# Optimization experiments

Measured on AMD Instinct MI355X. Metric: run time of the kernel, lower is better.

The kernel has to match this reference:

```python
import jax, jax.numpy as jnp
import numpy as np

TOTAL = 819200   # total flattened labels
BATCH = 16384    # number of samples (segments)
DIM = 128        # embed_dim
LABELS_PER = 50  # constant segment length (TOTAL = BATCH * LABELS_PER)


def setup_inputs() -> dict:
    key = jax.random.key(0)
    k_emb, k_w1, k_b1, k_w2, k_b2 = jax.random.split(key, 5)
    embeddings = jax.random.normal(k_emb, (TOTAL, DIM), dtype=jnp.float32)
    # weight_net params (PyTorch nn.Linear default-ish init scale)
    s1 = 1.0 / np.sqrt(DIM)
    W1 = jax.random.uniform(k_w1, (DIM, DIM), jnp.float32, -s1, s1)
    b1 = jax.random.uniform(k_b1, (DIM,), jnp.float32, -s1, s1)
    W2 = jax.random.uniform(k_w2, (DIM, 1), jnp.float32, -s1, s1)
    b2 = jax.random.uniform(k_b2, (1,), jnp.float32, -s1, s1)
    lengths = jnp.full((BATCH,), LABELS_PER, dtype=jnp.int32)
    return {"embeddings": embeddings, "W1": W1, "b1": b1, "W2": W2, "b2": b2,
            "lengths": lengths}


def reference(embeddings, W1, b1, W2, b2, lengths):
    # MLP scorer: Linear -> ReLU -> Linear -> Softmax(dim=0) (GLOBAL over all labels)
    h = jnp.maximum(embeddings @ W1 + b1, 0.0)           # (T, D)
    scores = h @ W2 + b2                                  # (T, 1)
    weights = jax.nn.softmax(scores, axis=0)              # (T, 1) global softmax
    # Ragged per-segment weighted sum via segment_sum
    batch = lengths.shape[0]
    total = embeddings.shape[0]
    seg_ids = jnp.repeat(jnp.arange(batch, dtype=jnp.int32), lengths,
                         total_repeat_length=total)       # (T,)
    pooled = jax.ops.segment_sum(embeddings * weights, seg_ids,
                                 num_segments=batch)      # (B, D)
    return pooled
```

## Files before the change

kernel.cpp:

```cpp
#include <hip/hip_runtime.h>
#include <hip/hip_bf16.h>
#include <math.h>

#define DIM 128

typedef __attribute__((ext_vector_type(8))) short bf16x8;
typedef __attribute__((ext_vector_type(4))) float f32x4;

union FragU { bf16x8 v; __hip_bfloat162 h[4]; };

static __device__ __forceinline__ ushort f2bf(float f) {
    unsigned u = __float_as_uint(f);
    u += 0x7FFFu + ((u >> 16) & 1u);
    return (ushort)(u >> 16);
}

typedef __attribute__((address_space(1))) const unsigned GASp;
typedef __attribute__((address_space(3))) unsigned LASp;
static __device__ __forceinline__ void gll16(const void* g, void* l) {
    __builtin_amdgcn_global_load_lds((GASp*)g, (LASp*)l, 16, 0, 0);
}

static __device__ __forceinline__ void stage16(float* buf, const float* emb,
                                               long row0, long Tm1, int lane) {
    #pragma unroll
    for (int i = 0; i < 8; ++i) {
        int s = i * 64 + lane;
        int r = s >> 5, x = s & 31;
        long gr = row0 + r; gr = (gr > Tm1) ? Tm1 : gr;
        gll16(emb + gr * 128 + ((x ^ (r & 7)) << 2), (char*)buf + i * 1024);
    }
}

__global__ __launch_bounds__(1024) void scan_kernel(const int* __restrict__ lengths,
                                                    int* __restrict__ offsets, int batch,
                                                    int* __restrict__ uniflag) {
    __shared__ int tsum[1024];
    __shared__ int ok;
    int tid = threadIdx.x;
    if (tid == 0) ok = 1;
    int L0 = lengths[0];
    int per = (batch + 1023) >> 10;
    int start = tid * per;
    int s = 0;
    int loc = 1;
    for (int i = 0; i < per; ++i) {
        int idx = start + i;
        if (idx < batch) {
            int l = lengths[idx];
            s += l;
            if (l != L0) loc = 0;
        }
    }
    tsum[tid] = s;
    __syncthreads();
    if (!loc) atomicAnd(&ok, 0);
    for (int off = 1; off < 1024; off <<= 1) {
        int v = (tid >= off) ? tsum[tid - off] : 0;
        __syncthreads();
        tsum[tid] += v;
        __syncthreads();
    }
    int base = (tid == 0) ? 0 : tsum[tid - 1];
    for (int i = 0; i < per; ++i) {
        int idx = start + i;
        if (idx < batch) { offsets[idx] = base; base += lengths[idx]; }
    }
    __syncthreads();
    if (tid == 0) uniflag[0] = ok;
}

static __device__ __forceinline__ void chunk_body(
        const float* __restrict__ bufc, int cv, int lane, int lr, int lg,
        int xc, int xh, const bf16x8 (&bfrag)[8][4],
        const float (&b1r)[8], const float (&w2r)[8],
        float& r_ref, float& Sp, float& t0, float& t1) {
    bf16x8 a[4];
    #pragma unroll
    for (int kc = 0; kc < 4; ++kc) {
        int c0 = kc * 8 + lg * 2;
        float4 q0 = *(const float4*)&bufc[(lr * 32 + (c0 ^ (lr & 7))) * 4];
        float4 q1 = *(const float4*)&bufc[(lr * 32 + ((c0 + 1) ^ (lr & 7))) * 4];
        FragU f;
        f.h[0] = __float22bfloat162_rn(make_float2(q0.x, q0.y));
        f.h[1] = __float22bfloat162_rn(make_float2(q0.z, q0.w));
        f.h[2] = __float22bfloat162_rn(make_float2(q1.x, q1.y));
        f.h[3] = __float22bfloat162_rn(make_float2(q1.z, q1.w));
        a[kc] = f.v;
    }

    f32x4 acc[8];
    #pragma unroll
    for (int ct = 0; ct < 8; ++ct) acc[ct] = (f32x4)(0.f);
    #pragma unroll
    for (int ct = 0; ct < 8; ++ct)
        #pragma unroll
        for (int kc = 0; kc < 4; ++kc)
            acc[ct] = __builtin_amdgcn_mfma_f32_16x16x32_bf16(a[kc], bfrag[ct][kc], acc[ct], 0, 0, 0);

    float p[4];
    #pragma unroll
    for (int reg = 0; reg < 4; ++reg) {
        float s = 0.f;
        #pragma unroll
        for (int ct = 0; ct < 8; ++ct) {
            float h = acc[ct][reg] + b1r[ct];
            h = fmaxf(h, 0.f);
            s = fmaf(h, w2r[ct], s);
        }
        p[reg] = s;
    }
    #pragma unroll
    for (int m = 1; m < 16; m <<= 1) {
        #pragma unroll
        for (int reg = 0; reg < 4; ++reg)
            p[reg] += __shfl_xor(p[reg], m, 64);
    }
    int r3 = lane & 3;
    float pr = p[0];
    pr = (r3 == 1) ? p[1] : pr;
    pr = (r3 == 2) ? p[2] : pr;
    pr = (r3 == 3) ? p[3] : pr;
    int src = ((lane & 12) << 2) + r3;
    float sv = __shfl(pr, src, 64);

    float s_l = (lr < cv) ? sv : -INFINITY;

    if (!__all(s_l - r_ref <= 8.f)) {
        float m_c = s_l;
        #pragma unroll
        for (int o = 1; o < 16; o <<= 1) m_c = fmaxf(m_c, __shfl_xor(m_c, o, 64));
        float r_new = fmaxf(r_ref, m_c);
        float scl = __expf(r_ref - r_new);
        Sp *= scl; t0 *= scl; t1 *= scl;
        r_ref = r_new;
    }
    float w_l = __expf(s_l - r_ref);
    Sp += w_l;

    #pragma unroll
    for (int jg = 0; jg < 4; ++jg) {
        int j0 = jg * 4;
        float2 e0 = *(const float2*)&bufc[((j0 + 0) * 32 + (xc ^ ((j0 + 0) & 7))) * 4 + xh * 2];
        float2 e1 = *(const float2*)&bufc[((j0 + 1) * 32 + (xc ^ ((j0 + 1) & 7))) * 4 + xh * 2];
        float2 e2 = *(const float2*)&bufc[((j0 + 2) * 32 + (xc ^ ((j0 + 2) & 7))) * 4 + xh * 2];
        float2 e3 = *(const float2*)&bufc[((j0 + 3) * 32 + (xc ^ ((j0 + 3) & 7))) * 4 + xh * 2];
        float w0 = __uint_as_float(__builtin_amdgcn_readlane(__float_as_uint(w_l), j0 + 0));
        float w1v = __uint_as_float(__builtin_amdgcn_readlane(__float_as_uint(w_l), j0 + 1));
        float w2v = __uint_as_float(__builtin_amdgcn_readlane(__float_as_uint(w_l), j0 + 2));
        float w3 = __uint_as_float(__builtin_amdgcn_readlane(__float_as_uint(w_l), j0 + 3));
        t0 = fmaf(w0, e0.x, t0); t1 = fmaf(w0, e0.y, t1);
        t0 = fmaf(w1v, e1.x, t0); t1 = fmaf(w1v, e1.y, t1);
        t0 = fmaf(w2v, e2.x, t0); t1 = fmaf(w2v, e2.y, t1);
        t0 = fmaf(w3, e3.x, t0); t1 = fmaf(w3, e3.y, t1);
    }
}

__global__ __launch_bounds__(256, 2) void fused_kernel(
        const float* __restrict__ emb, const float* __restrict__ W1,
        const float* __restrict__ b1, const float* __restrict__ W2,
        const float* __restrict__ b2, const int* __restrict__ offsets,
        const int* __restrict__ lengths, int batch, int T,
        const int* __restrict__ uniflag,
        float* __restrict__ mArr, float* __restrict__ sArr,
        float* __restrict__ tvec) {
    __shared__ __align__(16) char smem[65536];

    int tid = threadIdx.x;
    int lane = tid & 63;
    int wv = tid >> 6;
    int lr = lane & 15;
    int lg = lane >> 4;

    ushort* sB = (ushort*)smem;
    for (int i = 0; i < 16; ++i) {
        int q = tid + i * 256;
        int n = q >> 5;
        int k4 = q & 31;
        ushort4 w;
        w.x = f2bf(W1[(k4 * 4 + 0) * DIM + n]);
        w.y = f2bf(W1[(k4 * 4 + 1) * DIM + n]);
        w.z = f2bf(W1[(k4 * 4 + 2) * DIM + n]);
        w.w = f2bf(W1[(k4 * 4 + 3) * DIM + n]);
        int c = k4 >> 1;
        int a16 = n * 128 + ((c ^ (n & 7)) * 8) + (k4 & 1) * 4;
        *(ushort4*)&sB[a16] = w;
    }
    __syncthreads();
    bf16x8 bfrag[8][4];
    #pragma unroll
    for (int ct = 0; ct < 8; ++ct) {
        int n = ct * 16 + lr;
        #pragma unroll
        for (int kc = 0; kc < 4; ++kc) {
            int c = lg + kc * 4;
            bfrag[ct][kc] = *(const bf16x8*)&sB[n * 128 + ((c ^ (n & 7)) * 8)];
        }
    }
    float b1r[8], w2r[8];
    #pragma unroll
    for (int ct = 0; ct < 8; ++ct) {
        b1r[ct] = b1[ct * 16 + lr];
        w2r[ct] = W2[ct * 16 + lr];
    }
    __syncthreads();

    float* buf0 = (float*)(smem + wv * 16384);
    float* buf1 = (float*)(smem + wv * 16384 + 8192);

    long Tm1 = (long)T - 1;
    int nwaves = gridDim.x * 4;
    int gwave = blockIdx.x * 4 + wv;
    int per = (batch + nwaves - 1) / nwaves;
    int seg0 = gwave * per;
    int segend = seg0 + per; if (segend > batch) segend = batch;
    if (seg0 >= segend) return;

    int xc = lane >> 1, xh = lane & 1;
    int uni = __builtin_amdgcn_readfirstlane(uniflag[0]);

    if (uni) {
        int L = __builtin_amdgcn_readfirstlane(lengths[0]);
        int nch = (L + 15) >> 4;
        int ss = seg0, sc = 0;
        #pragma unroll
        for (int k = 0; k < 2; ++k) {
            if (ss < segend) {
                stage16(k ? buf1 : buf0, emb, (long)ss * L + sc * 16, Tm1, lane);
                if (++sc == nch) { sc = 0; ++ss; }
            }
        }
        int cur = 0;
        for (int seg = seg0; seg < segend; ++seg) {
            float r_ref = -INFINITY, Sp = 0.f, t0 = 0.f, t1 = 0.f;
            for (int c = 0; c < nch; ++c) {
                if (seg == segend - 1 && c == nch - 1)
                    asm volatile("s_waitcnt vmcnt(0)" ::: "memory");
                else
                    asm volatile("s_waitcnt vmcnt(8)" ::: "memory");
                float* bufc = cur ? buf1 : buf0;
                chunk_body(bufc, L - c * 16, lane, lr, lg, xc, xh,
                           bfrag, b1r, w2r, r_ref, Sp, t0, t1);
                asm volatile("s_waitcnt lgkmcnt(0)" ::: "memory");
                if (ss < segend) {
                    stage16(bufc, emb, (long)ss * L + sc * 16, Tm1, lane);
                    if (++sc == nch) { sc = 0; ++ss; }
                }
                cur ^= 1;
            }
            #pragma unroll
            for (int o = 1; o < 16; o <<= 1) Sp += __shfl_xor(Sp, o, 64);
            *(float2*)&tvec[(long)seg * DIM + 2 * lane] = make_float2(t0, t1);
            if (lane == 0) { mArr[seg] = r_ref; sArr[seg] = Sp; }
        }
    } else {
        for (int seg = seg0; seg < segend; ++seg) {
            long off = offsets[seg];
            int len = lengths[seg];
            int nch = (len + 15) >> 4;
            float r_ref = -INFINITY, Sp = 0.f, t0 = 0.f, t1 = 0.f;

            if (nch > 0) stage16(buf0, emb, off, Tm1, lane);
            if (nch > 1) stage16(buf1, emb, off + 16, Tm1, lane);

            for (int c = 0; c < nch; ++c) {
                float* bufc = (c & 1) ? buf1 : buf0;
                if (c + 1 < nch) asm volatile("s_waitcnt vmcnt(8)" ::: "memory");
                else             asm volatile("s_waitcnt vmcnt(0)" ::: "memory");
                chunk_body(bufc, len - c * 16, lane, lr, lg, xc, xh,
                           bfrag, b1r, w2r, r_ref, Sp, t0, t1);
                asm volatile("s_waitcnt lgkmcnt(0)" ::: "memory");
                if (c + 2 < nch) stage16(bufc, emb, off + (long)(c + 2) * 16, Tm1, lane);
            }
            #pragma unroll
            for (int o = 1; o < 16; o <<= 1) Sp += __shfl_xor(Sp, o, 64);
            *(float2*)&tvec[(long)seg * DIM + 2 * lane] = make_float2(t0, t1);
            if (lane == 0) { mArr[seg] = r_ref; sArr[seg] = Sp; }
        }
    }
}

__global__ __launch_bounds__(1024) void segreduce_kernel(const float* __restrict__ mArr,
        const float* __restrict__ sArr, int batch, float* __restrict__ stats) {
    __shared__ float redm[16], reds[16];
    int tid = threadIdx.x;
    int wave = tid >> 6, ln = tid & 63;
    float m = -INFINITY;
    for (int i = tid; i < batch; i += 1024) m = fmaxf(m, mArr[i]);
    #pragma unroll
    for (int o = 32; o >= 1; o >>= 1) m = fmaxf(m, __shfl_xor(m, o, 64));
    if (ln == 0) redm[wave] = m;
    __syncthreads();
    float M = -INFINITY;
    #pragma unroll
    for (int k = 0; k < 16; ++k) M = fmaxf(M, redm[k]);
    float s = 0.f;
    for (int i = tid; i < batch; i += 1024) s += sArr[i] * expf(mArr[i] - M);
    #pragma unroll
    for (int o = 32; o >= 1; o >>= 1) s += __shfl_xor(s, o, 64);
    if (ln == 0) reds[wave] = s;
    __syncthreads();
    if (tid == 0) {
        float S = 0.f;
        #pragma unroll
        for (int k = 0; k < 16; ++k) S += reds[k];
        stats[0] = M;
        stats[1] = 1.0f / S;
    }
}

__global__ __launch_bounds__(256) void scale_kernel(const float* __restrict__ tvec,
        const float* __restrict__ mArr, const float* __restrict__ stats,
        float* __restrict__ out, int n) {
    int idx = blockIdx.x * 256 + threadIdx.x;
    if (idx >= n) return;
    float M = stats[0], invS = stats[1];
    int b = idx >> 7;
    out[idx] = tvec[idx] * (expf(mArr[b] - M) * invS);
}

extern "C" void kernel_launch(void* const* d_in, const int* in_sizes, int n_in,
                              void* d_out, int out_size, void* d_ws, size_t ws_size,
                              hipStream_t stream) {
    const float* emb     = (const float*)d_in[0];
    const float* W1      = (const float*)d_in[1];
    const float* b1      = (const float*)d_in[2];
    const float* W2      = (const float*)d_in[3];
    const float* b2      = (const float*)d_in[4];
    const int*   lengths = (const int*)d_in[5];
    int T = in_sizes[0] / DIM;
    int batch = in_sizes[5];
    float* out = (float*)d_out;

    int*   offsets = (int*)d_ws;
    float* mArr    = (float*)(offsets + batch);
    float* sArr    = mArr + batch;
    float* stats   = sArr + batch;
    int*   uniflag = (int*)(stats + 2);
    float* tvec    = stats + 4;

    scan_kernel<<<1, 1024, 0, stream>>>(lengths, offsets, batch, uniflag);
    fused_kernel<<<512, 256, 0, stream>>>(emb, W1, b1, W2, b2, offsets, lengths,
                                          batch, T, uniflag, mArr, sArr, tvec);
    segreduce_kernel<<<1, 1024, 0, stream>>>(mArr, sArr, batch, stats);
    scale_kernel<<<(out_size + 255) / 256, 256, 0, stream>>>(tvec, mArr, stats, out, out_size);
}
```

Before: 163.6 us.

## Pool from bf16 MFMA fragments in registers and prefetch next chunk earlier

Pooling now reuses the bf16 A-fragments already loaded for the MFMA and keeps a per-lane 4x8 partial accumulator, instead of re-reading fp32 rows from LDS each chunk. Partials are reduced with cross-lane shuffles once per segment. The next chunk's LDS prefetch is issued right after the fragment reads so it overlaps with the MFMA and softmax work. This trades LDS traffic for more registers and shuffles, and the pooled sum now uses bf16-rounded embeddings, which reduces accuracy.

```diff
diff --git a/kernel.cpp b/kernel.cpp
--- a/kernel.cpp
+++ b/kernel.cpp
@@ -71,10 +71,11 @@
 }
 
 static __device__ __forceinline__ void chunk_body(
-        const float* __restrict__ bufc, int cv, int lane, int lr, int lg,
-        int xc, int xh, const bf16x8 (&bfrag)[8][4],
+        float* __restrict__ bufc, int cv, int lane, int lr, int lg,
+        long stage_row, const float* __restrict__ emb, long Tm1,
+        const bf16x8 (&bfrag)[8][4],
         const float (&b1r)[8], const float (&w2r)[8],
-        float& r_ref, float& Sp, float& t0, float& t1) {
+        float& r_ref, float& Sp, float (&pool)[4][8]) {
     bf16x8 a[4];
     #pragma unroll
     for (int kc = 0; kc < 4; ++kc) {
@@ -88,6 +89,8 @@
         f.h[3] = __float22bfloat162_rn(make_float2(q1.z, q1.w));
         a[kc] = f.v;
     }
+    asm volatile("s_waitcnt lgkmcnt(0)" ::: "memory");
+    if (stage_row >= 0) stage16(bufc, emb, stage_row, Tm1, lane);
 
     f32x4 acc[8];
     #pragma unroll
@@ -132,28 +135,51 @@
         for (int o = 1; o < 16; o <<= 1) m_c = fmaxf(m_c, __shfl_xor(m_c, o, 64));
         float r_new = fmaxf(r_ref, m_c);
         float scl = __expf(r_ref - r_new);
-        Sp *= scl; t0 *= scl; t1 *= scl;
+        Sp *= scl;
+        #pragma unroll
+        for (int kc = 0; kc < 4; ++kc)
+            #pragma unroll
+            for (int k = 0; k < 8; ++k) pool[kc][k] *= scl;
         r_ref = r_new;
     }
     float w_l = __expf(s_l - r_ref);
     Sp += w_l;
 
     #pragma unroll
-    for (int jg = 0; jg < 4; ++jg) {
-        int j0 = jg * 4;
-        float2 e0 = *(const float2*)&bufc[((j0 + 0) * 32 + (xc ^ ((j0 + 0) & 7))) * 4 + xh * 2];
-        float2 e1 = *(const float2*)&bufc[((j0 + 1) * 32 + (xc ^ ((j0 + 1) & 7))) * 4 + xh * 2];
-        float2 e2 = *(const float2*)&bufc[((j0 + 2) * 32 + (xc ^ ((j0 + 2) & 7))) * 4 + xh * 2];
-        float2 e3 = *(const float2*)&bufc[((j0 + 3) * 32 + (xc ^ ((j0 + 3) & 7))) * 4 + xh * 2];
-        float w0 = __uint_as_float(__builtin_amdgcn_readlane(__float_as_uint(w_l), j0 + 0));
-        float w1v = __uint_as_float(__builtin_amdgcn_readlane(__float_as_uint(w_l), j0 + 1));
-        float w2v = __uint_as_float(__builtin_amdgcn_readlane(__float_as_uint(w_l), j0 + 2));
-        float w3 = __uint_as_float(__builtin_amdgcn_readlane(__float_as_uint(w_l), j0 + 3));
-        t0 = fmaf(w0, e0.x, t0); t1 = fmaf(w0, e0.y, t1);
-        t0 = fmaf(w1v, e1.x, t0); t1 = fmaf(w1v, e1.y, t1);
-        t0 = fmaf(w2v, e2.x, t0); t1 = fmaf(w2v, e2.y, t1);
-        t0 = fmaf(w3, e3.x, t0); t1 = fmaf(w3, e3.y, t1);
-    }
+    for (int kc = 0; kc < 4; ++kc) {
+        FragU fa; fa.v = a[kc];
+        #pragma unroll
+        for (int i = 0; i < 4; ++i) {
+            float2 e = __bfloat1622float2(fa.h[i]);
+            pool[kc][2 * i]     = fmaf(w_l, e.x, pool[kc][2 * i]);
+            pool[kc][2 * i + 1] = fmaf(w_l, e.y, pool[kc][2 * i + 1]);
+        }
+    }
+}
+
+static __device__ __forceinline__ void seg_finalize(
+        int seg, int lane, int lr, int lg, float r_ref, float Sp,
+        float (&pool)[4][8], float* __restrict__ mArr, float* __restrict__ sArr,
+        float* __restrict__ tvec) {
+    #pragma unroll
+    for (int o = 1; o < 16; o <<= 1) Sp += __shfl_xor(Sp, o, 64);
+    #pragma unroll
+    for (int o = 1; o < 16; o <<= 1) {
+        #pragma unroll
+        for (int kc = 0; kc < 4; ++kc)
+            #pragma unroll
+            for (int k = 0; k < 8; ++k)
+                pool[kc][k] += __shfl_xor(pool[kc][k], o, 64);
+    }
+    if (lr == 0) {
+        float* tb = &tvec[(long)seg * DIM + lg * 8];
+        #pragma unroll
+        for (int kc = 0; kc < 4; ++kc) {
+            *(float4*)(tb + kc * 32)     = make_float4(pool[kc][0], pool[kc][1], pool[kc][2], pool[kc][3]);
+            *(float4*)(tb + kc * 32 + 4) = make_float4(pool[kc][4], pool[kc][5], pool[kc][6], pool[kc][7]);
+        }
+    }
+    if (lane == 0) { mArr[seg] = r_ref; sArr[seg] = Sp; }
 }
 
 __global__ __launch_bounds__(256, 2) void fused_kernel(
@@ -216,7 +242,6 @@
     int segend = seg0 + per; if (segend > batch) segend = batch;
     if (seg0 >= segend) return;
 
-    int xc = lane >> 1, xh = lane & 1;
     int uni = __builtin_amdgcn_readfirstlane(uniflag[0]);
 
     if (uni) {
@@ -232,33 +257,41 @@
         }
         int cur = 0;
         for (int seg = seg0; seg < segend; ++seg) {
-            float r_ref = -INFINITY, Sp = 0.f, t0 = 0.f, t1 = 0.f;
+            float r_ref = -INFINITY, Sp = 0.f;
+            float pool[4][8];
+            #pragma unroll
+            for (int kc = 0; kc < 4; ++kc)
+                #pragma unroll
+                for (int k = 0; k < 8; ++k) pool[kc][k] = 0.f;
+
             for (int c = 0; c < nch; ++c) {
                 if (seg == segend - 1 && c == nch - 1)
                     asm volatile("s_waitcnt vmcnt(0)" ::: "memory");
                 else
                     asm volatile("s_waitcnt vmcnt(8)" ::: "memory");
                 float* bufc = cur ? buf1 : buf0;
-                chunk_body(bufc, L - c * 16, lane, lr, lg, xc, xh,
-                           bfrag, b1r, w2r, r_ref, Sp, t0, t1);
-                asm volatile("s_waitcnt lgkmcnt(0)" ::: "memory");
+                long stage_row = -1;
                 if (ss < segend) {
-                    stage16(bufc, emb, (long)ss * L + sc * 16, Tm1, lane);
+                    stage_row = (long)ss * L + sc * 16;
                     if (++sc == nch) { sc = 0; ++ss; }
                 }
+                chunk_body(bufc, L - c * 16, lane, lr, lg, stage_row, emb, Tm1,
+                           bfrag, b1r, w2r, r_ref, Sp, pool);
                 cur ^= 1;
             }
-            #pragma unroll
-            for (int o = 1; o < 16; o <<= 1) Sp += __shfl_xor(Sp, o, 64);
-            *(float2*)&tvec[(long)seg * DIM + 2 * lane] = make_float2(t0, t1);
-            if (lane == 0) { mArr[seg] = r_ref; sArr[seg] = Sp; }
+            seg_finalize(seg, lane, lr, lg, r_ref, Sp, pool, mArr, sArr, tvec);
         }
     } else {
         for (int seg = seg0; seg < segend; ++seg) {
             long off = offsets[seg];
             int len = lengths[seg];
             int nch = (len + 15) >> 4;
-            float r_ref = -INFINITY, Sp = 0.f, t0 = 0.f, t1 = 0.f;
+            float r_ref = -INFINITY, Sp = 0.f;
+            float pool[4][8];
+            #pragma unroll
+            for (int kc = 0; kc < 4; ++kc)
+                #pragma unroll
+                for (int k = 0; k < 8; ++k) pool[kc][k] = 0.f;
 
             if (nch > 0) stage16(buf0, emb, off, Tm1, lane);
             if (nch > 1) stage16(buf1, emb, off + 16, Tm1, lane);
@@ -267,15 +300,11 @@
                 float* bufc = (c & 1) ? buf1 : buf0;
                 if (c + 1 < nch) asm volatile("s_waitcnt vmcnt(8)" ::: "memory");
                 else             asm volatile("s_waitcnt vmcnt(0)" ::: "memory");
-                chunk_body(bufc, len - c * 16, lane, lr, lg, xc, xh,
-                           bfrag, b1r, w2r, r_ref, Sp, t0, t1);
-                asm volatile("s_waitcnt lgkmcnt(0)" ::: "memory");
-                if (c + 2 < nch) stage16(bufc, emb, off + (long)(c + 2) * 16, Tm1, lane);
+                long stage_row = (c + 2 < nch) ? (off + (long)(c + 2) * 16) : -1;
+                chunk_body(bufc, len - c * 16, lane, lr, lg, stage_row, emb, Tm1,
+                           bfrag, b1r, w2r, r_ref, Sp, pool);
             }
-            #pragma unroll
-            for (int o = 1; o < 16; o <<= 1) Sp += __shfl_xor(Sp, o, 64);
-            *(float2*)&tvec[(long)seg * DIM + 2 * lane] = make_float2(t0, t1);
-            if (lane == 0) { mArr[seg] = r_ref; sArr[seg] = Sp; }
+            seg_finalize(seg, lane, lr, lg, r_ref, Sp, pool, mArr, sArr, tvec);
         }
     }
 }
```

New measurement: 250.9 us. 53.4% more time.
